# Performance work log

Hardware: AMD Instinct MI355X
Metric: run time of the kernel (lower is better)

Reference implementation:

```python
import jax, jax.numpy as jnp
import numpy as np

B, C, D, H, W = 2, 128, 32, 64, 64  # ch_in=128, shurink=0 -> Cs = ch_out = C
Cs = C


def setup_inputs() -> dict:
    key = jax.random.key(0)
    ks = jax.random.split(key, 9)
    std = 1.0 / np.sqrt(C).astype(np.float32)
    x = jax.random.normal(ks[0], (B, C, D, H, W), jnp.float32)
    Wk = jax.random.normal(ks[1], (Cs, C), jnp.float32) * std
    bk = jax.random.normal(ks[2], (Cs,), jnp.float32) * std
    Wq = jax.random.normal(ks[3], (Cs, C), jnp.float32) * std
    bq = jax.random.normal(ks[4], (Cs,), jnp.float32) * std
    Wv = jax.random.normal(ks[5], (Cs, C), jnp.float32) * std
    bv = jax.random.normal(ks[6], (Cs,), jnp.float32) * std
    Wo = jax.random.normal(ks[7], (C, Cs), jnp.float32) * (1.0 / np.sqrt(Cs).astype(np.float32))
    bo = jax.random.normal(ks[8], (C,), jnp.float32) * std
    return {"x": x, "Wk": Wk, "bk": bk, "Wq": Wq, "bq": bq, "Wv": Wv, "bv": bv, "Wo": Wo, "bo": bo}


def reference(x, Wk, bk, Wq, bq, Wv, bv, Wo, bo):
    # 1x1x1 Conv3d == per-voxel linear over channels
    def proj(Wt, bt):
        return jnp.einsum('bcdhw,oc->bodhw', x, Wt) + bt[None, :, None, None, None]

    K = proj(Wk, bk)  # [B,Cs,D,H,W]
    Q = proj(Wq, bq)
    V = proj(Wv, bv)

    scale = 1.0 / jnp.sqrt(jnp.asarray(Cs, x.dtype))
    # per-pixel depth attention: scores[b,h,w,i,j] = sum_c K[b,c,i,h,w] * Q[b,c,j,h,w]
    scores = jnp.einsum('bcihw,bcjhw->bhwij', K, Q) * scale
    # torch softmax dim=1 on [N,D,D] == key-position axis i (axis=-2 here)
    A = jax.nn.softmax(scores, axis=-2)
    # a[b,c,j,h,w] = sum_i V[b,c,i,h,w] * A[b,h,w,i,j]  (== bmm(V, A))
    a = jnp.einsum('bcihw,bhwij->bcjhw', V, A)
    out = jnp.einsum('bcjhw,oc->bojhw', a, Wo) + bo[None, :, None, None, None]
    return x + out  # atten_factor = 1
```

## Files before the change

### kernel.cpp

```cpp
#include <hip/hip_runtime.h>

typedef _Float16 f16x8 __attribute__((ext_vector_type(8)));
typedef _Float16 f16x4 __attribute__((ext_vector_type(4)));
typedef float    f32x4 __attribute__((ext_vector_type(4)));

#define MFMA(a,b,c) __builtin_amdgcn_mfma_f32_16x16x32_f16((a),(b),(c),0,0,0)


__global__ __launch_bounds__(128) void prep_kernel(
    const float* __restrict__ Wk, const float* __restrict__ bk,
    const float* __restrict__ Wq, const float* __restrict__ bq,
    const float* __restrict__ Wv, const float* __restrict__ bv,
    const float* __restrict__ Wo, const float* __restrict__ bo,
    _Float16* __restrict__ wh, float* __restrict__ bf) {
  __shared__ float worow[128];
  const int o = blockIdx.x;
  const int c = threadIdx.x;
  const float scale = 0.08838834764831844f;
  worow[c] = Wo[o*128 + c];
  __syncthreads();
  float acc = 0.f, a2 = 0.f;
  for (int m = 0; m < 128; ++m) {
    acc += worow[m] * Wv[m*128 + c];
    a2  += worow[m] * bv[m];
  }
  wh[o*128+c]         = (_Float16)(Wk[o*128+c] * scale);
  wh[16384 + o*128+c] = (_Float16)(Wq[o*128+c]);
  wh[32768 + o*128+c] = (_Float16)acc;
  if (c == 0) {
    bf[o]       = bk[o] * scale;
    bf[128 + o] = bq[o];
    bf[256 + o] = a2 + bo[o];
  }
}

__global__ __launch_bounds__(256) void transpose_kernel(
    const float* __restrict__ x, _Float16* __restrict__ Xg) {
  __shared__ _Float16 Lt[64 * 130];
  const int bid = blockIdx.x;
  const int h = bid & 63, d = (bid >> 6) & 31, b = bid >> 11;
  const int tid = threadIdx.x;
  const size_t rbase = (size_t)b*16777216u + (size_t)d*4096 + h*64;
#pragma unroll
  for (int i = 0; i < 8; ++i) {
    const int chunk = tid + i*256;
    const int c = chunk >> 4, wq = chunk & 15;
    const f32x4 v = *(const f32x4*)(x + rbase + (size_t)c*131072 + wq*4);
    Lt[(wq*4+0)*130 + c] = (_Float16)v[0];
    Lt[(wq*4+1)*130 + c] = (_Float16)v[1];
    Lt[(wq*4+2)*130 + c] = (_Float16)v[2];
    Lt[(wq*4+3)*130 + c] = (_Float16)v[3];
  }
  __syncthreads();
  const int gbase = b*1024 + h*16;
#pragma unroll
  for (int i = 0; i < 4; ++i) {
    const int idx = tid + i*256;
    const int w = idx >> 4, ck = (idx & 15) * 8;
    const int wg = w >> 2, p = w & 3;
    const f16x8 v = *(const f16x8*)(Lt + w*130 + ck);
    *(f16x8*)(Xg + (size_t)(gbase + wg)*16384 + (p*32 + d)*128 + ck) = v;
  }
}

__device__ __forceinline__ f16x4 cvt4(f32x4 v, f32x4 b) {
  f16x4 r;
  r[0] = (_Float16)(v[0] + b[0]); r[1] = (_Float16)(v[1] + b[1]);
  r[2] = (_Float16)(v[2] + b[2]); r[3] = (_Float16)(v[3] + b[3]);
  return r;
}
__device__ __forceinline__ f16x4 cvt4z(f32x4 v) {
  f16x4 r;
  r[0] = (_Float16)v[0]; r[1] = (_Float16)v[1];
  r[2] = (_Float16)v[2]; r[3] = (_Float16)v[3];
  return r;
}

__global__ __launch_bounds__(1024) void attn_kernel(
    const _Float16* __restrict__ Xg, const _Float16* __restrict__ wh,
    const float* __restrict__ bfp, float* __restrict__ out) {
  __shared__ __align__(16) char lds[133120];
  _Float16* Xt = (_Float16*)(lds);
  _Float16* Kt = (_Float16*)(lds + 34816);
  _Float16* Qt = (_Float16*)(lds + 69632);
  float*    Sm = (float*)(lds + 104448);
  _Float16* At = (_Float16*)(lds + 122880);
  float*    ot = (float*)(lds + 34816);

  const int tid  = threadIdx.x;
  const int lane = tid & 63;
  const int wv   = tid >> 6;
  const int quad = lane >> 4;
  const int l15  = lane & 15;
  const int mi   = wv & 7;
  const int ni   = wv >> 3;

  const int bid = blockIdx.x;
  const int g = (bid & ~31) | ((bid & 7) << 2) | ((bid >> 3) & 3);
  const int b   = g >> 10;
  const int rem = g & 1023;
  const int h   = rem >> 4;
  const int wg  = rem & 15;
  const size_t pbase = (size_t)b * 16777216u + (size_t)(h*64 + wg*4);

  f16x8 wk[4], wq[4], wp[4];
  {
    const int wrow = (mi*16 + l15) * 128;
#pragma unroll
    for (int kk = 0; kk < 4; ++kk) {
      const int off = wrow + kk*32 + quad*8;
      wk[kk] = *(const f16x8*)(wh + off);
      wq[kk] = *(const f16x8*)(wh + 16384 + off);
      wp[kk] = *(const f16x8*)(wh + 32768 + off);
    }
  }
  const f32x4 bk4 = *(const f32x4*)(bfp +       mi*16 + quad*4);
  const f32x4 bq4 = *(const f32x4*)(bfp + 128 + mi*16 + quad*4);
  const f32x4 bp4 = *(const f32x4*)(bfp + 256 + mi*16 + quad*4);
  const f32x4 zz = {0.f, 0.f, 0.f, 0.f};

  {
    const _Float16* src = Xg + (size_t)g * 16384;
#pragma unroll
    for (int i = 0; i < 2; ++i) {
      const int idx = tid + i*1024;
      const int row = idx >> 4, ck = (idx & 15) * 8;
      const f16x8 v = *(const f16x8*)(src + row*128 + ck);
      *(f16x8*)(Xt + row*136 + ck) = v;
    }
  }
  __syncthreads();

  {
    f32x4 aK[4] = {zz, zz, zz, zz};
    f32x4 aQ[4] = {zz, zz, zz, zz};
#pragma unroll
    for (int kk = 0; kk < 4; ++kk) {
      const int co = kk*32 + quad*8;
      f16x8 bfv[4];
#pragma unroll
      for (int nt = 0; nt < 4; ++nt)
        bfv[nt] = *(const f16x8*)(Xt + (ni*64 + nt*16 + l15)*136 + co);
#pragma unroll
      for (int nt = 0; nt < 4; ++nt) {
        aK[nt] = MFMA(wk[kk], bfv[nt], aK[nt]);
        aQ[nt] = MFMA(wq[kk], bfv[nt], aQ[nt]);
      }
    }
#pragma unroll
    for (int nt = 0; nt < 4; ++nt) {
      const int ad = (ni*64 + nt*16 + l15)*136 + mi*16 + quad*4;
      *(f16x4*)(Kt + ad) = cvt4(aK[nt], bk4);
      *(f16x4*)(Qt + ad) = cvt4(aQ[nt], bq4);
    }
  }
  __syncthreads();

  {
    const int p = wv >> 2, ti = (wv >> 1) & 1, tj = wv & 1;
    f32x4 aS = zz;
#pragma unroll
    for (int kk = 0; kk < 4; ++kk) {
      const int co = kk*32 + quad*8;
      const f16x8 ak  = *(const f16x8*)(Kt + (p*32 + ti*16 + l15)*136 + co);
      const f16x8 bq_ = *(const f16x8*)(Qt + (p*32 + tj*16 + l15)*136 + co);
      aS = MFMA(ak, bq_, aS);
    }
    *(f32x4*)(Sm + (p*32 + tj*16 + l15)*36 + ti*16 + quad*4) = aS;
  }
  __syncthreads();

  if (tid < 128) {
    const float* srow = Sm + tid*36;
    float mx = srow[0];
#pragma unroll
    for (int i = 1; i < 32; ++i) mx = fmaxf(mx, srow[i]);
    float den = 0.f;
#pragma unroll
    for (int i = 0; i < 32; ++i) den += __expf(srow[i] - mx);
    const float rr = 1.0f / den;
    _Float16* arow = At + tid*40;
#pragma unroll
    for (int i = 0; i < 32; ++i) arow[i] = (_Float16)(__expf(srow[i] - mx) * rr);
  }
  __syncthreads();

  {
    const int p = wv & 3, mg = wv >> 2;
    f16x8 bA[2];
#pragma unroll
    for (int tj = 0; tj < 2; ++tj)
      bA[tj] = *(const f16x8*)(At + (p*32 + tj*16 + l15)*40 + quad*8);
#pragma unroll
    for (int t2 = 0; t2 < 2; ++t2) {
      const int ms = mg*2 + t2;
      const int cbase = (p*32 + quad*8)*136 + ms*16 + l15;
      const f16x8 ax = { Xt[cbase], Xt[cbase+136], Xt[cbase+272], Xt[cbase+408],
                         Xt[cbase+544], Xt[cbase+680], Xt[cbase+816], Xt[cbase+952] };
#pragma unroll
      for (int tj = 0; tj < 2; ++tj) {
        f32x4 aU = MFMA(ax, bA[tj], zz);
        *(f16x4*)(Kt + (p*32 + tj*16 + l15)*136 + ms*16 + quad*4) = cvt4z(aU);
      }
    }
  }
  __syncthreads();

  f32x4 aO[4] = {zz, zz, zz, zz};
#pragma unroll
  for (int kk = 0; kk < 4; ++kk) {
    const int co = kk*32 + quad*8;
    f16x8 bfv[4];
#pragma unroll
    for (int nt = 0; nt < 4; ++nt)
      bfv[nt] = *(const f16x8*)(Kt + (ni*64 + nt*16 + l15)*136 + co);
#pragma unroll
    for (int nt = 0; nt < 4; ++nt)
      aO[nt] = MFMA(wp[kk], bfv[nt], aO[nt]);
  }
  __syncthreads();

#pragma unroll
  for (int nt = 0; nt < 4; ++nt) {
    const int col = ni*64 + nt*16 + l15;
    const int pp = col >> 5, jj = col & 31;
    float* dst = ot + (mi*16 + quad*4)*132 + jj*4 + pp;
    dst[0]   = aO[nt][0] + bp4[0];
    dst[132] = aO[nt][1] + bp4[1];
    dst[264] = aO[nt][2] + bp4[2];
    dst[396] = aO[nt][3] + bp4[3];
  }
  __syncthreads();

#pragma unroll
  for (int it = 0; it < 4; ++it) {
    const int o = it*32 + (tid >> 5);
    const int j = tid & 31;
    f32x4 v = *(const f32x4*)(ot + o*132 + j*4);
    v[0] += (float)Xt[(0*32 + j)*136 + o];
    v[1] += (float)Xt[(1*32 + j)*136 + o];
    v[2] += (float)Xt[(2*32 + j)*136 + o];
    v[3] += (float)Xt[(3*32 + j)*136 + o];
    *(f32x4*)(out + pbase + (size_t)o*131072 + j*4096) = v;
  }
}

extern "C" void kernel_launch(void* const* d_in, const int* in_sizes, int n_in,
                              void* d_out, int out_size, void* d_ws, size_t ws_size,
                              hipStream_t stream) {
  const float* x  = (const float*)d_in[0];
  const float* Wk = (const float*)d_in[1];
  const float* bk = (const float*)d_in[2];
  const float* Wq = (const float*)d_in[3];
  const float* bq = (const float*)d_in[4];
  const float* Wv = (const float*)d_in[5];
  const float* bv = (const float*)d_in[6];
  const float* Wo = (const float*)d_in[7];
  const float* bo = (const float*)d_in[8];
  float* out = (float*)d_out;
  _Float16* wh = (_Float16*)d_ws;
  float* bf = (float*)((char*)d_ws + 98304);
  _Float16* Xg = (_Float16*)((char*)d_ws + 131072);

  prep_kernel<<<dim3(128), dim3(128), 0, stream>>>(Wk, bk, Wq, bq, Wv, bv, Wo, bo, wh, bf);
  transpose_kernel<<<dim3(4096), dim3(256), 0, stream>>>(x, Xg);
  attn_kernel<<<dim3(2048), dim3(1024), 0, stream>>>(Xg, wh, bf, out);
}
```

Baseline: 380.1 us.

## Fold K and Q projections into one bilinear matrix and drop softmax-invariant terms

Precomputes M = Wk^T Wq (scaled) so the scores become X^T (M X) plus a per-key term u·x_i. Terms that are constant along the softmax axis (bk and bq·bk contributions) are dropped. This removes one projection GEMM per block and shrinks LDS from about 130KB to about 80KB, which may allow two blocks per CU. It also parallelises the softmax across 8 lanes per row with shuffles, removes the shared-memory staging before the output store, seeds the accumulator with the residual, and makes the transpose kernel register-only. The trade-off is that scores are rounded to fp16 before the softmax.

After: 436.6 us. +14.9%, slower.

```diff
diff --git a/kernel.cpp b/kernel.cpp
--- a/kernel.cpp
+++ b/kernel.cpp
@@ -8,67 +8,59 @@
 
 
 __global__ __launch_bounds__(128) void prep_kernel(
-    const float* __restrict__ Wk, const float* __restrict__ bk,
-    const float* __restrict__ Wq, const float* __restrict__ bq,
-    const float* __restrict__ Wv, const float* __restrict__ bv,
-    const float* __restrict__ Wo, const float* __restrict__ bo,
+    const float* __restrict__ Wk, const float* __restrict__ bq_,
+    const float* __restrict__ Wq, const float* __restrict__ Wv,
+    const float* __restrict__ bv, const float* __restrict__ Wo,
+    const float* __restrict__ bo,
     _Float16* __restrict__ wh, float* __restrict__ bf) {
-  __shared__ float worow[128];
-  const int o = blockIdx.x;
+  __shared__ float ckl[128], rol[128];
+  const int r = blockIdx.x;
   const int c = threadIdx.x;
   const float scale = 0.08838834764831844f;
-  worow[c] = Wo[o*128 + c];
-  __syncthreads();
-  float acc = 0.f, a2 = 0.f;
-  for (int m = 0; m < 128; ++m) {
-    acc += worow[m] * Wv[m*128 + c];
-    a2  += worow[m] * bv[m];
-  }
-  wh[o*128+c]         = (_Float16)(Wk[o*128+c] * scale);
-  wh[16384 + o*128+c] = (_Float16)(Wq[o*128+c]);
-  wh[32768 + o*128+c] = (_Float16)acc;
-  if (c == 0) {
-    bf[o]       = bk[o] * scale;
-    bf[128 + o] = bq[o];
-    bf[256 + o] = a2 + bo[o];
+  ckl[c] = Wk[c*128 + r];
+  rol[c] = Wo[r*128 + c];
+  __syncthreads();
+  float aM = 0.f, aV = 0.f, a2 = 0.f;
+  for (int o = 0; o < 128; ++o) {
+    aM += ckl[o] * Wq[o*128 + c];
+    aV += rol[o] * Wv[o*128 + c];
+    a2 += rol[o] * bv[o];
+  }
+  wh[r*128 + c]         = (_Float16)(aM * scale);
+  wh[16384 + r*128 + c] = (_Float16)aV;
+  if (c == 0) bf[r] = a2 + bo[r];
+  if (r == 0) {
+    float au = 0.f;
+    for (int o = 0; o < 128; ++o) au += Wk[o*128 + c] * bq_[o];
+    bf[128 + c] = au * scale;
   }
 }
 
 __global__ __launch_bounds__(256) void transpose_kernel(
     const float* __restrict__ x, _Float16* __restrict__ Xg) {
-  __shared__ _Float16 Lt[64 * 130];
   const int bid = blockIdx.x;
   const int h = bid & 63, d = (bid >> 6) & 31, b = bid >> 11;
-  const int tid = threadIdx.x;
-  const size_t rbase = (size_t)b*16777216u + (size_t)d*4096 + h*64;
-#pragma unroll
-  for (int i = 0; i < 8; ++i) {
-    const int chunk = tid + i*256;
-    const int c = chunk >> 4, wq = chunk & 15;
-    const f32x4 v = *(const f32x4*)(x + rbase + (size_t)c*131072 + wq*4);
-    Lt[(wq*4+0)*130 + c] = (_Float16)v[0];
-    Lt[(wq*4+1)*130 + c] = (_Float16)v[1];
-    Lt[(wq*4+2)*130 + c] = (_Float16)v[2];
-    Lt[(wq*4+3)*130 + c] = (_Float16)v[3];
-  }
-  __syncthreads();
+  const int t = threadIdx.x;
+  const int cg = t & 15, wq = t >> 4;
+  const size_t rbase = (size_t)b*16777216u + (size_t)d*4096 + h*64 + wq*4;
   const int gbase = b*1024 + h*16;
-#pragma unroll
-  for (int i = 0; i < 4; ++i) {
-    const int idx = tid + i*256;
-    const int w = idx >> 4, ck = (idx & 15) * 8;
-    const int wg = w >> 2, p = w & 3;
-    const f16x8 v = *(const f16x8*)(Lt + w*130 + ck);
-    *(f16x8*)(Xg + (size_t)(gbase + wg)*16384 + (p*32 + d)*128 + ck) = v;
-  }
-}
-
-__device__ __forceinline__ f16x4 cvt4(f32x4 v, f32x4 b) {
-  f16x4 r;
-  r[0] = (_Float16)(v[0] + b[0]); r[1] = (_Float16)(v[1] + b[1]);
-  r[2] = (_Float16)(v[2] + b[2]); r[3] = (_Float16)(v[3] + b[3]);
-  return r;
-}
+  _Float16* dst0 = Xg + (size_t)(gbase + wq)*16384 + d*128;
+#pragma unroll
+  for (int i = 0; i < 2; ++i) {
+    f32x4 v[4];
+#pragma unroll
+    for (int cc = 0; cc < 4; ++cc)
+      v[cc] = *(const f32x4*)(x + rbase + (size_t)(cg*4 + cc + 64*i)*131072u);
+#pragma unroll
+    for (int r = 0; r < 4; ++r) {
+      f16x4 o;
+      o[0] = (_Float16)v[0][r]; o[1] = (_Float16)v[1][r];
+      o[2] = (_Float16)v[2][r]; o[3] = (_Float16)v[3][r];
+      *(f16x4*)(dst0 + r*4096 + cg*4 + 64*i) = o;
+    }
+  }
+}
+
 __device__ __forceinline__ f16x4 cvt4z(f32x4 v) {
   f16x4 r;
   r[0] = (_Float16)v[0]; r[1] = (_Float16)v[1];
@@ -76,16 +68,14 @@
   return r;
 }
 
-__global__ __launch_bounds__(1024) void attn_kernel(
+__global__ __launch_bounds__(1024, 8) void attn_kernel(
     const _Float16* __restrict__ Xg, const _Float16* __restrict__ wh,
     const float* __restrict__ bfp, float* __restrict__ out) {
-  __shared__ __align__(16) char lds[133120];
+  __shared__ __align__(16) char lds[80384];
   _Float16* Xt = (_Float16*)(lds);
-  _Float16* Kt = (_Float16*)(lds + 34816);
-  _Float16* Qt = (_Float16*)(lds + 69632);
-  float*    Sm = (float*)(lds + 104448);
-  _Float16* At = (_Float16*)(lds + 122880);
-  float*    ot = (float*)(lds + 34816);
+  _Float16* Yt = (_Float16*)(lds + 34816);
+  _Float16* SA = (_Float16*)(lds + 69632);
+  float*    al = (float*)(lds + 79872);
 
   const int tid  = threadIdx.x;
   const int lane = tid & 63;
@@ -103,22 +93,20 @@
   const int wg  = rem & 15;
   const size_t pbase = (size_t)b * 16777216u + (size_t)(h*64 + wg*4);
 
-  f16x8 wk[4], wq[4], wp[4];
+  f16x8 wm[4], wp[4];
   {
     const int wrow = (mi*16 + l15) * 128;
 #pragma unroll
     for (int kk = 0; kk < 4; ++kk) {
       const int off = wrow + kk*32 + quad*8;
-      wk[kk] = *(const f16x8*)(wh + off);
-      wq[kk] = *(const f16x8*)(wh + 16384 + off);
-      wp[kk] = *(const f16x8*)(wh + 32768 + off);
-    }
-  }
-  const f32x4 bk4 = *(const f32x4*)(bfp +       mi*16 + quad*4);
-  const f32x4 bq4 = *(const f32x4*)(bfp + 128 + mi*16 + quad*4);
-  const f32x4 bp4 = *(const f32x4*)(bfp + 256 + mi*16 + quad*4);
+      wm[kk] = *(const f16x8*)(wh + off);
+      wp[kk] = *(const f16x8*)(wh + 16384 + off);
+    }
+  }
+  const f32x4 bp4 = *(const f32x4*)(bfp + mi*16 + quad*4);
   const f32x4 zz = {0.f, 0.f, 0.f, 0.f};
 
+  if (tid < 128) ((float*)SA)[tid] = bfp[128 + tid];
   {
     const _Float16* src = Xg + (size_t)g * 16384;
 #pragma unroll
@@ -132,8 +120,19 @@
   __syncthreads();
 
   {
-    f32x4 aK[4] = {zz, zz, zz, zz};
-    f32x4 aQ[4] = {zz, zz, zz, zz};
+    const int n = tid >> 3, sub = tid & 7;
+    const float* us = (const float*)SA;
+    const f16x8 x0 = *(const f16x8*)(Xt + n*136 + sub*16);
+    const f16x8 x1 = *(const f16x8*)(Xt + n*136 + sub*16 + 8);
+    float a = 0.f;
+#pragma unroll
+    for (int k = 0; k < 8; ++k) a += (float)x0[k] * us[sub*16 + k];
+#pragma unroll
+    for (int k = 0; k < 8; ++k) a += (float)x1[k] * us[sub*16 + 8 + k];
+    a += __shfl_xor(a, 1); a += __shfl_xor(a, 2); a += __shfl_xor(a, 4);
+    if (sub == 0) al[n] = a;
+
+    f32x4 aY[4] = {zz, zz, zz, zz};
 #pragma unroll
     for (int kk = 0; kk < 4; ++kk) {
       const int co = kk*32 + quad*8;
@@ -142,17 +141,12 @@
       for (int nt = 0; nt < 4; ++nt)
         bfv[nt] = *(const f16x8*)(Xt + (ni*64 + nt*16 + l15)*136 + co);
 #pragma unroll
-      for (int nt = 0; nt < 4; ++nt) {
-        aK[nt] = MFMA(wk[kk], bfv[nt], aK[nt]);
-        aQ[nt] = MFMA(wq[kk], bfv[nt], aQ[nt]);
-      }
-    }
-#pragma unroll
-    for (int nt = 0; nt < 4; ++nt) {
-      const int ad = (ni*64 + nt*16 + l15)*136 + mi*16 + quad*4;
-      *(f16x4*)(Kt + ad) = cvt4(aK[nt], bk4);
-      *(f16x4*)(Qt + ad) = cvt4(aQ[nt], bq4);
-    }
+      for (int nt = 0; nt < 4; ++nt)
+        aY[nt] = MFMA(wm[kk], bfv[nt], aY[nt]);
+    }
+#pragma unroll
+    for (int nt = 0; nt < 4; ++nt)
+      *(f16x4*)(Yt + (ni*64 + nt*16 + l15)*136 + mi*16 + quad*4) = cvt4z(aY[nt]);
   }
   __syncthreads();
 
@@ -162,26 +156,33 @@
 #pragma unroll
     for (int kk = 0; kk < 4; ++kk) {
       const int co = kk*32 + quad*8;
-      const f16x8 ak  = *(const f16x8*)(Kt + (p*32 + ti*16 + l15)*136 + co);
-      const f16x8 bq_ = *(const f16x8*)(Qt + (p*32 + tj*16 + l15)*136 + co);
-      aS = MFMA(ak, bq_, aS);
-    }
-    *(f32x4*)(Sm + (p*32 + tj*16 + l15)*36 + ti*16 + quad*4) = aS;
-  }
-  __syncthreads();
-
-  if (tid < 128) {
-    const float* srow = Sm + tid*36;
-    float mx = srow[0];
-#pragma unroll
-    for (int i = 1; i < 32; ++i) mx = fmaxf(mx, srow[i]);
-    float den = 0.f;
-#pragma unroll
-    for (int i = 0; i < 32; ++i) den += __expf(srow[i] - mx);
+      const f16x8 ax = *(const f16x8*)(Xt + (p*32 + ti*16 + l15)*136 + co);
+      const f16x8 by = *(const f16x8*)(Yt + (p*32 + tj*16 + l15)*136 + co);
+      aS = MFMA(ax, by, aS);
+    }
+    *(f16x4*)(SA + (p*32 + tj*16 + l15)*40 + ti*16 + quad*4) = cvt4z(aS);
+  }
+  __syncthreads();
+
+  {
+    const int n = tid >> 3, sub = tid & 7, p = n >> 5;
+    f16x4 sv = *(const f16x4*)(SA + n*40 + sub*4);
+    float s[4];
+#pragma unroll
+    for (int k = 0; k < 4; ++k) s[k] = (float)sv[k] + al[p*32 + sub*4 + k];
+    float mx = fmaxf(fmaxf(s[0], s[1]), fmaxf(s[2], s[3]));
+    mx = fmaxf(mx, __shfl_xor(mx, 1));
+    mx = fmaxf(mx, __shfl_xor(mx, 2));
+    mx = fmaxf(mx, __shfl_xor(mx, 4));
+    float e[4], den = 0.f;
+#pragma unroll
+    for (int k = 0; k < 4; ++k) { e[k] = __expf(s[k] - mx); den += e[k]; }
+    den += __shfl_xor(den, 1); den += __shfl_xor(den, 2); den += __shfl_xor(den, 4);
     const float rr = 1.0f / den;
-    _Float16* arow = At + tid*40;
-#pragma unroll
-    for (int i = 0; i < 32; ++i) arow[i] = (_Float16)(__expf(srow[i] - mx) * rr);
+    f16x4 av;
+#pragma unroll
+    for (int k = 0; k < 4; ++k) av[k] = (_Float16)(e[k] * rr);
+    *(f16x4*)(SA + n*40 + sub*4) = av;
   }
   __syncthreads();
 
@@ -190,7 +191,7 @@
     f16x8 bA[2];
 #pragma unroll
     for (int tj = 0; tj < 2; ++tj)
-      bA[tj] = *(const f16x8*)(At + (p*32 + tj*16 + l15)*40 + quad*8);
+      bA[tj] = *(const f16x8*)(SA + (p*32 + tj*16 + l15)*40 + quad*8);
 #pragma unroll
     for (int t2 = 0; t2 < 2; ++t2) {
       const int ms = mg*2 + t2;
@@ -200,48 +201,44 @@
 #pragma unroll
       for (int tj = 0; tj < 2; ++tj) {
         f32x4 aU = MFMA(ax, bA[tj], zz);
-        *(f16x4*)(Kt + (p*32 + tj*16 + l15)*136 + ms*16 + quad*4) = cvt4z(aU);
+        *(f16x4*)(Yt + (p*32 + tj*16 + l15)*136 + ms*16 + quad*4) = cvt4z(aU);
       }
     }
   }
   __syncthreads();
 
-  f32x4 aO[4] = {zz, zz, zz, zz};
-#pragma unroll
-  for (int kk = 0; kk < 4; ++kk) {
-    const int co = kk*32 + quad*8;
-    f16x8 bfv[4];
-#pragma unroll
-    for (int nt = 0; nt < 4; ++nt)
-      bfv[nt] = *(const f16x8*)(Kt + (ni*64 + nt*16 + l15)*136 + co);
-#pragma unroll
-    for (int nt = 0; nt < 4; ++nt)
-      aO[nt] = MFMA(wp[kk], bfv[nt], aO[nt]);
-  }
-  __syncthreads();
-
-#pragma unroll
-  for (int nt = 0; nt < 4; ++nt) {
-    const int col = ni*64 + nt*16 + l15;
-    const int pp = col >> 5, jj = col & 31;
-    float* dst = ot + (mi*16 + quad*4)*132 + jj*4 + pp;
-    dst[0]   = aO[nt][0] + bp4[0];
-    dst[132] = aO[nt][1] + bp4[1];
-    dst[264] = aO[nt][2] + bp4[2];
-    dst[396] = aO[nt][3] + bp4[3];
-  }
-  __syncthreads();
-
-#pragma unroll
-  for (int it = 0; it < 4; ++it) {
-    const int o = it*32 + (tid >> 5);
-    const int j = tid & 31;
-    f32x4 v = *(const f32x4*)(ot + o*132 + j*4);
-    v[0] += (float)Xt[(0*32 + j)*136 + o];
-    v[1] += (float)Xt[(1*32 + j)*136 + o];
-    v[2] += (float)Xt[(2*32 + j)*136 + o];
-    v[3] += (float)Xt[(3*32 + j)*136 + o];
-    *(f32x4*)(out + pbase + (size_t)o*131072 + j*4096) = v;
+  {
+    f32x4 aO[4];
+#pragma unroll
+    for (int nt = 0; nt < 4; ++nt) {
+      const int base = (ni*64 + nt*16 + l15)*136 + mi*16 + quad*4;
+#pragma unroll
+      for (int r = 0; r < 4; ++r)
+        aO[nt][r] = bp4[r] + (float)Xt[base + r];
+    }
+#pragma unroll
+    for (int kk = 0; kk < 4; ++kk) {
+      const int co = kk*32 + quad*8;
+      f16x8 bfv[4];
+#pragma unroll
+      for (int nt = 0; nt < 4; ++nt)
+        bfv[nt] = *(const f16x8*)(Yt + (ni*64 + nt*16 + l15)*136 + co);
+#pragma unroll
+      for (int nt = 0; nt < 4; ++nt)
+        aO[nt] = MFMA(wp[kk], bfv[nt], aO[nt]);
+    }
+#pragma unroll
+    for (int ntp = 0; ntp < 2; ++ntp) {
+      const int n = ni*64 + ntp*16 + l15;
+      const int j = n & 31, p0 = n >> 5;
+      const size_t rowb = pbase + (size_t)j*4096 + p0;
+#pragma unroll
+      for (int r = 0; r < 4; ++r) {
+        const int o = mi*16 + quad*4 + r;
+        float2 v2 = make_float2(aO[ntp][r], aO[ntp+2][r]);
+        *(float2*)(out + rowb + (size_t)o*131072u) = v2;
+      }
+    }
   }
 }
 
@@ -250,7 +247,6 @@
                               hipStream_t stream) {
   const float* x  = (const float*)d_in[0];
   const float* Wk = (const float*)d_in[1];
-  const float* bk = (const float*)d_in[2];
   const float* Wq = (const float*)d_in[3];
   const float* bq = (const float*)d_in[4];
   const float* Wv = (const float*)d_in[5];
@@ -259,10 +255,10 @@
   const float* bo = (const float*)d_in[8];
   float* out = (float*)d_out;
   _Float16* wh = (_Float16*)d_ws;
-  float* bf = (float*)((char*)d_ws + 98304);
+  float* bf = (float*)((char*)d_ws + 65536);
   _Float16* Xg = (_Float16*)((char*)d_ws + 131072);
 
-  prep_kernel<<<dim3(128), dim3(128), 0, stream>>>(Wk, bk, Wq, bq, Wv, bv, Wo, bo, wh, bf);
+  prep_kernel<<<dim3(128), dim3(128), 0, stream>>>(Wk, bq, Wq, Wv, bv, Wo, bo, wh, bf);
   transpose_kernel<<<dim3(4096), dim3(256), 0, stream>>>(x, Xg);
   attn_kernel<<<dim3(2048), dim3(1024), 0, stream>>>(Xg, wh, bf, out);
 }
```
